# Kernel optimization log

Hardware: AMD Instinct MI355X
Metric: run time of the kernel (lower is better)

The kernel has to match this reference:

```python
import jax, jax.numpy as jnp
import numpy as np

B, S, D = 2, 2048, 2048
NH, NKV, HD = 16, 4, 128
REP = NH // NKV
EPS = 1e-6
ROPE_THETA = 1e6


def setup_inputs() -> dict:
    key = jax.random.key(0)
    ks = jax.random.split(key, 6)
    x = jax.random.normal(ks[0], (B, S, D), jnp.float32)
    # real rotary embeddings: [S, HD]
    inv_freq = 1.0 / (ROPE_THETA ** (np.arange(0, HD, 2, dtype=np.float64) / HD))
    freqs = np.outer(np.arange(S, dtype=np.float64), inv_freq)
    emb = np.concatenate([freqs, freqs], axis=-1)
    cos = jnp.asarray(np.cos(emb), jnp.float32)
    sin = jnp.asarray(np.sin(emb), jnp.float32)
    scale = 1.0 / np.sqrt(D)
    Wq = jax.random.normal(ks[1], (D, NH * HD), jnp.float32) * scale   # [in, out]
    Wk = jax.random.normal(ks[2], (D, NKV * HD), jnp.float32) * scale
    Wv = jax.random.normal(ks[3], (D, NKV * HD), jnp.float32) * scale
    Wo = jax.random.normal(ks[4], (NH * HD, D), jnp.float32) * (1.0 / np.sqrt(NH * HD))
    q_norm_w = jnp.ones((HD,), jnp.float32)
    k_norm_w = jnp.ones((HD,), jnp.float32)
    return dict(x=x, cos=cos, sin=sin, Wq=Wq, Wk=Wk, Wv=Wv, Wo=Wo,
                q_norm_w=q_norm_w, k_norm_w=k_norm_w)


def _rms_norm(h, w):
    var = jnp.mean(h * h, axis=-1, keepdims=True)
    return w * (h * jax.lax.rsqrt(var + EPS))


def _rotate_half(h):
    h1, h2 = jnp.split(h, 2, axis=-1)
    return jnp.concatenate([-h2, h1], axis=-1)


def reference(x, cos, sin, Wq, Wk, Wv, Wo, q_norm_w, k_norm_w):
    b, s, _ = x.shape
    q = (x @ Wq).reshape(b, s, NH, HD)
    k = (x @ Wk).reshape(b, s, NKV, HD)
    v = (x @ Wv).reshape(b, s, NKV, HD)
    # per-head QK RMSNorm
    q = _rms_norm(q, q_norm_w)
    k = _rms_norm(k, k_norm_w)
    # RoPE: cos/sin [S,HD] -> broadcast over batch and heads
    c = cos[None, :, None, :]
    s_ = sin[None, :, None, :]
    q = q * c + _rotate_half(q) * s_
    k = k * c + _rotate_half(k) * s_
    # GQA: group q heads per kv head instead of materializing repeat_kv
    qg = q.reshape(b, s, NKV, REP, HD)
    scores = jnp.einsum('bqgrd,bkgd->bgrqk', qg, k) / np.sqrt(HD)
    causal = jnp.tril(jnp.ones((s, s), bool))  # [q,k]
    scores = jnp.where(causal, scores, -jnp.inf)
    probs = jax.nn.softmax(scores.astype(jnp.float32), axis=-1).astype(q.dtype)
    out = jnp.einsum('bgrqk,bkgd->bqgrd', probs, v).reshape(b, s, NH * HD)
    return out @ Wo
```

## Files before the change

kernel.cpp:

```cpp
#include <hip/hip_runtime.h>
#include <hip/hip_bf16.h>
#include <math.h>

#define B_ 2
#define S_ 2048
#define D_ 2048
#define NH_ 16
#define NKV_ 4
#define HD_ 128
#define EPS_ 1e-6f
#define SCALE_ 0.08838834764831845f
#define LOG2E_ 1.4426950408889634f
#define KOFF_ 2048
#define VOFF_ 2560

typedef float f32x4 __attribute__((ext_vector_type(4)));
typedef short bf16x8 __attribute__((ext_vector_type(8)));
typedef short short4v __attribute__((ext_vector_type(4)));
typedef float float4v __attribute__((ext_vector_type(4)));
typedef unsigned uint2v __attribute__((ext_vector_type(2)));
typedef unsigned uint4v __attribute__((ext_vector_type(4)));

static __device__ __forceinline__ short f2bf(float f) {
    union { float f; unsigned u; } x{f};
    unsigned r = (x.u + 0x7fff + ((x.u >> 16) & 1)) >> 16;
    return (short)r;
}
static __device__ __forceinline__ float bf2f(short s) {
    union { unsigned u; float f; } x; x.u = ((unsigned)(unsigned short)s) << 16; return x.f;
}
static __device__ __forceinline__ unsigned pack_bf2(float a, float b) {
    return __builtin_amdgcn_perm(__builtin_bit_cast(unsigned, b),
                                 __builtin_bit_cast(unsigned, a), 0x07060302u);
}

#define AS1(p) ((const __attribute__((address_space(1))) void*)(p))
#define AS3(p) ((__attribute__((address_space(3))) void*)(p))
static __device__ __forceinline__ void async16(const void* g, void* l) {
    __builtin_amdgcn_global_load_lds(AS1(g), AS3(l), 16, 0, 0);
}

__global__ __launch_bounds__(256) void cast_kernel(const float* __restrict__ in,
                                                   short* __restrict__ out) {
    size_t i = ((size_t)blockIdx.x * 256 + threadIdx.x) * 4;
    float4v v = *(const float4v*)(in + i);
    short4v o; o.x = f2bf(v.x); o.y = f2bf(v.y); o.z = f2bf(v.z); o.w = f2bf(v.w);
    *(short4v*)(out + i) = o;
}

__global__ __launch_bounds__(256) void transpose_all_kernel(const float* __restrict__ Wq,
                                                            const float* __restrict__ Wk,
                                                            const float* __restrict__ Wv,
                                                            const float* __restrict__ Wo,
                                                            short* __restrict__ Wt,
                                                            short* __restrict__ Wot) {
    __shared__ float tile[64][65];
    const int bx = blockIdx.x, by = blockIdx.y;
    const float* src; short* dst; int N, nb;
    if (bx < 32)      { src = Wq; dst = Wt;                         N = 2048; nb = bx; }
    else if (bx < 40) { src = Wk; dst = Wt + (size_t)KOFF_ * 2048;  N = 512;  nb = bx - 32; }
    else if (bx < 48) { src = Wv; dst = Wt + (size_t)VOFF_ * 2048;  N = 512;  nb = bx - 40; }
    else              { src = Wo; dst = Wot;                        N = 2048; nb = bx - 48; }
    const int n0 = nb * 64, k0 = by * 64;
    const int tid = threadIdx.x;
    for (int r = 0; r < 16; ++r) {
        int k = r * 4 + (tid >> 6);
        int n = tid & 63;
        tile[k][n] = src[(size_t)(k0 + k) * N + n0 + n];
    }
    __syncthreads();
    for (int r = 0; r < 4; ++r) {
        int n  = r * 16 + (tid >> 4);
        int kk = (tid & 15) * 4;
        short4v o4;
        o4.x = f2bf(tile[kk + 0][n]); o4.y = f2bf(tile[kk + 1][n]);
        o4.z = f2bf(tile[kk + 2][n]); o4.w = f2bf(tile[kk + 3][n]);
        *(short4v*)&dst[(size_t)(n0 + n) * 2048 + k0 + kk] = o4;
    }
}

template<typename TC>
__global__ __launch_bounds__(256) void gemm_tt_kernel(const short* __restrict__ A,
                                                      const short* __restrict__ Bt,
                                                      TC* __restrict__ C,
                                                      int M, int N, int K) {
    __shared__ short As[128 * 32];
    __shared__ short Bs[128 * 32];

    const int tid  = threadIdx.x;
    const int bn   = blockIdx.x, bm = blockIdx.y;
    const int wave = tid >> 6, lane = tid & 63;
    const int quad = lane >> 4, l16 = lane & 15;
    const int wr = wave >> 1, wc = wave & 1;

    f32x4 acc[4][4];
    for (int i = 0; i < 4; ++i)
        for (int j = 0; j < 4; ++j) acc[i][j] = (f32x4){0.f, 0.f, 0.f, 0.f};

    const short* Abase = A  + (size_t)(bm * 128) * K;
    const short* Bbase = Bt + (size_t)(bn * 128) * K;

    int ci0 = wave * 128 + lane;
    for (int k0 = 0; k0 < K; k0 += 32) {
        __syncthreads();
        for (int t = 0; t < 2; ++t) {
            int ci = ci0 + t * 64;
            int r  = ci >> 2;
            int c  = ((ci & 3) - (r >> 1)) & 3;
            size_t goff = (size_t)r * K + k0 + c * 8;
            async16(Abase + goff, &As[ci * 8]);
            async16(Bbase + goff, &Bs[ci * 8]);
        }
        __syncthreads();

        bf16x8 af[4], bfv[4];
        for (int mt = 0; mt < 4; ++mt) {
            int r = wr * 64 + mt * 16 + l16;
            af[mt] = *(const bf16x8*)&As[r * 32 + (((quad + (r >> 1)) & 3) * 8)];
        }
        for (int nt = 0; nt < 4; ++nt) {
            int r = wc * 64 + nt * 16 + l16;
            bfv[nt] = *(const bf16x8*)&Bs[r * 32 + (((quad + (r >> 1)) & 3) * 8)];
        }
        for (int mt = 0; mt < 4; ++mt)
            for (int nt = 0; nt < 4; ++nt)
                acc[mt][nt] = __builtin_amdgcn_mfma_f32_16x16x32_bf16(
                    af[mt], bfv[nt], acc[mt][nt], 0, 0, 0);
    }

    for (int mt = 0; mt < 4; ++mt)
        for (int nt = 0; nt < 4; ++nt)
            for (int j = 0; j < 4; ++j) {
                int row = bm * 128 + wr * 64 + mt * 16 + quad * 4 + j;
                int col = bn * 128 + wc * 64 + nt * 16 + l16;
                float v = acc[mt][nt][j];
                if constexpr (__is_same(TC, short))
                    C[(size_t)row * N + col] = f2bf(v);
                else
                    C[(size_t)row * N + col] = v;
            }
}

#define QKV_ITERS 16

__global__ __launch_bounds__(512, 2) void qkv_fused_kernel(const short* __restrict__ xb,
                                                           const short* __restrict__ Wt,
                                                           const float* __restrict__ cosb,
                                                           const float* __restrict__ sinb,
                                                           const float* __restrict__ qw,
                                                           const float* __restrict__ kw,
                                                           short* __restrict__ q_rope,
                                                           short* __restrict__ k_rope,
                                                           short* __restrict__ vtr) {
    __shared__ __align__(16) short smem[65536];
    __shared__ float ss2[4][256];

    short* A0 = smem;
    short* A1 = smem + 16384;
    short* B0 = smem + 32768;
    short* B1 = smem + 49152;

    const int tid  = threadIdx.x;
    const int orig = blockIdx.y * 12 + blockIdx.x;
    const int swz  = (orig & 7) * 24 + (orig >> 3);
    const int bn = swz % 12, bm = swz / 12;
    const int wave = tid >> 6, lane = tid & 63;
    const int quad = lane >> 4, l16 = lane & 15;
    const int wr = wave >> 2, wc = wave & 3;

    const short* Ag = xb + (size_t)(bm * 256) * 2048;
    const short* Bg = Wt + (size_t)(bn * 256) * 2048;

    f32x4 acc[8][4];
#pragma unroll
    for (int i = 0; i < 8; ++i)
#pragma unroll
        for (int j = 0; j < 4; ++j) acc[i][j] = (f32x4){0.f, 0.f, 0.f, 0.f};

    bf16x8 a[4][2], b0[2][2], b1[2][2];

    auto stage_half = [&](const short* gpanel, int t, int h, short* lslot) {
#pragma unroll
        for (int u = 0; u < 2; ++u) {
            int ci = u * 512 + tid;
            int r  = ci >> 3;
            int cb = ((ci & 7) * 16) ^ ((r & 7) << 4);
            async16(gpanel + (size_t)(h * 128 + r) * 2048 + t * 64 + (cb >> 1),
                    lslot + h * 8192 + ci * 8);
        }
    };

#define LDA_(lbuf, qm) \
    _Pragma("unroll") for (int mt = 0; mt < 4; ++mt) \
    _Pragma("unroll") for (int ks = 0; ks < 2; ++ks) { \
        int row_ = wr * 128 + (qm) * 64 + mt * 16 + l16; \
        int cb_  = (ks * 64 + quad * 16) ^ ((row_ & 7) << 4); \
        a[mt][ks] = *(const bf16x8*)&(lbuf)[row_ * 64 + (cb_ >> 1)]; \
    }
#define LDB_(lbuf, qn, breg) \
    _Pragma("unroll") for (int ntl = 0; ntl < 2; ++ntl) \
    _Pragma("unroll") for (int ks = 0; ks < 2; ++ks) { \
        int row_ = wc * 64 + (qn) * 32 + ntl * 16 + l16; \
        int cb_  = (ks * 64 + quad * 16) ^ ((row_ & 7) << 4); \
        breg[ntl][ks] = *(const bf16x8*)&(lbuf)[row_ * 64 + (cb_ >> 1)]; \
    }
#define MFMA16_(qm, qn, breg) \
    _Pragma("unroll") for (int mt = 0; mt < 4; ++mt) \
    _Pragma("unroll") for (int ntl = 0; ntl < 2; ++ntl) \
    _Pragma("unroll") for (int ks = 0; ks < 2; ++ks) \
        acc[(qm) * 4 + mt][(qn) * 2 + ntl] = __builtin_amdgcn_mfma_f32_16x16x32_bf16( \
            a[mt][ks], breg[ntl][ks], acc[(qm) * 4 + mt][(qn) * 2 + ntl], 0, 0, 0);
#define PH_BAR() do { __builtin_amdgcn_sched_barrier(0); __builtin_amdgcn_s_barrier(); } while (0)
#define PH_MFMA2(qm) do { \
        __builtin_amdgcn_s_setprio(1); MFMA16_(qm, 0, b0); MFMA16_(qm, 1, b1); \
        __builtin_amdgcn_s_setprio(0); \
        __builtin_amdgcn_sched_barrier(0); __builtin_amdgcn_s_barrier(); } while (0)

    stage_half(Bg, 0, 0, B0); stage_half(Bg, 0, 1, B0);
    stage_half(Ag, 0, 0, A0); stage_half(Ag, 0, 1, A0);
    stage_half(Bg, 1, 0, B1); stage_half(Bg, 1, 1, B1);
    asm volatile("s_waitcnt vmcnt(4)" ::: "memory");
    __builtin_amdgcn_s_barrier();

#pragma unroll 1
    for (int i = 0; i < QKV_ITERS; ++i) {
        const int tE = 2 * i, tO = 2 * i + 1;
        const bool more = (i < QKV_ITERS - 1);

        LDA_(A0, 0); LDB_(B0, 0, b0); LDB_(B0, 1, b1);
        stage_half(Ag, tO, 0, A1); stage_half(Ag, tO, 1, A1);
        PH_BAR();
        PH_MFMA2(0);

        LDA_(A0, 1);
        if (more) {
            stage_half(Bg, tE + 2, 0, B0); stage_half(Bg, tE + 2, 1, B0);
            asm volatile("s_waitcnt vmcnt(4)" ::: "memory");
        } else {
            asm volatile("s_waitcnt vmcnt(0)" ::: "memory");
        }
        PH_BAR();
        PH_MFMA2(1);

        LDA_(A1, 0); LDB_(B1, 0, b0); LDB_(B1, 1, b1);
        if (more) { stage_half(Ag, tE + 2, 0, A0); stage_half(Ag, tE + 2, 1, A0); }
        PH_BAR();
        PH_MFMA2(0);

        LDA_(A1, 1);
        if (more) {
            stage_half(Bg, tO + 2, 0, B1); stage_half(Bg, tO + 2, 1, B1);
            asm volatile("s_waitcnt vmcnt(4)" ::: "memory");
        }
        PH_BAR();
        PH_MFMA2(1);
    }

    if (bn >= 10) {
        const int gbase = (bn - 10) * 2;
#pragma unroll
        for (int am = 0; am < 8; ++am) {
            int tok0 = bm * 256 + wr * 128 + am * 16 + quad * 4;
            int bb = tok0 >> 11, s0 = tok0 & (S_ - 1);
#pragma unroll
            for (int nt = 0; nt < 4; ++nt) {
                int col = wc * 64 + nt * 16 + l16;
                int g = gbase + (col >> 7);
                int d = col & 127;
                short4v o4;
                o4.x = f2bf(acc[am][nt][0]); o4.y = f2bf(acc[am][nt][1]);
                o4.z = f2bf(acc[am][nt][2]); o4.w = f2bf(acc[am][nt][3]);
                *(short4v*)&vtr[((size_t)(bb * NKV_ + g) * HD_ + d) * S_ + s0] = o4;
            }
        }
        return;
    }

    {
        float pss[8][4];
#pragma unroll
        for (int am = 0; am < 8; ++am)
#pragma unroll
            for (int j = 0; j < 4; ++j) {
                float s = 0.f;
#pragma unroll
                for (int nt = 0; nt < 4; ++nt) s += acc[am][nt][j] * acc[am][nt][j];
                pss[am][j] = s;
            }
#pragma unroll
        for (int off = 1; off < 16; off <<= 1)
#pragma unroll
            for (int am = 0; am < 8; ++am)
#pragma unroll
                for (int j = 0; j < 4; ++j)
                    pss[am][j] += __shfl_xor(pss[am][j], off);
        if (l16 == 0)
#pragma unroll
            for (int am = 0; am < 8; ++am)
#pragma unroll
                for (int j = 0; j < 4; ++j)
                    ss2[wc][wr * 128 + am * 16 + quad * 4 + j] = pss[am][j];
    }
    short* ct = smem;
#pragma unroll
    for (int am = 0; am < 8; ++am)
#pragma unroll
        for (int nt = 0; nt < 4; ++nt)
#pragma unroll
            for (int j = 0; j < 4; ++j)
                ct[(wr * 128 + am * 16 + quad * 4 + j) * 256 + wc * 64 + nt * 16 + l16]
                    = f2bf(acc[am][nt][j]);
    __syncthreads();

    const bool isQ = (bn < 8);
    const float osc = isQ ? (SCALE_ * LOG2E_) : 1.0f;
    const float* w = isQ ? qw : kw;
#pragma unroll 1
    for (int it = 0; it < 16; ++it) {
        int idx = it * 512 + tid;
        int row = idx >> 5;
        int s32 = idx & 31;
        int head = s32 >> 4, seg = s32 & 15;
        int tok = bm * 256 + row;
        int bb = tok >> 11, s = tok & (S_ - 1);
        float rstd = rsqrtf((ss2[2 * head][row] + ss2[2 * head + 1][row]) * (1.0f / HD_) + EPS_);
        int c0 = seg * 8, p0 = (seg ^ 8) * 8;
        bf16x8 ta = *(const bf16x8*)&ct[row * 256 + head * 128 + c0];
        bf16x8 tb = *(const bf16x8*)&ct[row * 256 + head * 128 + p0];
        float sgn = (seg < 8) ? -1.0f : 1.0f;
        float4v cs0 = *(const float4v*)&cosb[(size_t)s * HD_ + c0];
        float4v cs1 = *(const float4v*)&cosb[(size_t)s * HD_ + c0 + 4];
        float4v sn0 = *(const float4v*)&sinb[(size_t)s * HD_ + c0];
        float4v sn1 = *(const float4v*)&sinb[(size_t)s * HD_ + c0 + 4];
        float ov[8];
#pragma unroll
        for (int i = 0; i < 8; ++i) {
            float n1 = bf2f(ta[i]) * rstd * w[c0 + i];
            float n2 = bf2f(tb[i]) * rstd * w[p0 + i];
            float cs = (i < 4) ? cs0[i & 3] : cs1[i & 3];
            float sn = (i < 4) ? sn0[i & 3] : sn1[i & 3];
            ov[i] = (n1 * cs + sgn * n2 * sn) * osc;
        }
        uint4v wv;
#pragma unroll
        for (int i2 = 0; i2 < 4; ++i2)
            wv[i2] = ((unsigned)(unsigned short)f2bf(ov[2 * i2])) |
                     ((unsigned)(unsigned short)f2bf(ov[2 * i2 + 1]) << 16);
        int gh = isQ ? (bn * 2 + head) : ((bn - 8) * 2 + head);
        short* dst = isQ
            ? q_rope + ((size_t)(bb * S_ + s) * NH_ + gh) * HD_ + c0
            : k_rope + ((size_t)(bb * NKV_ + gh) * S_ + s) * HD_ + c0;
        *(uint4v*)dst = wv;
    }
#undef LDA_
#undef LDB_
#undef MFMA16_
#undef PH_BAR
#undef PH_MFMA2
}

__global__ __launch_bounds__(256, 2) void attn_kernel(const short* __restrict__ qr,
                                                      const short* __restrict__ kg,
                                                      const short* __restrict__ vt,
                                                      short* __restrict__ aout) {
    __shared__ short Ks[2][64 * 128];
    __shared__ short Vs[2][128 * 64];

    const int lin = blockIdx.x;
    const int b  = lin & 1;
    const int g  = (lin >> 1) & 3;
    const int hq = (lin >> 3) & 3;
    const int pr = lin >> 5;
    const int h  = g * 4 + hq;

    const int wave = threadIdx.x >> 6, lane = threadIdx.x & 63;
    const int quad = lane >> 4, l16 = lane & 15;

    const short* kbase = kg + (size_t)(b * NKV_ + g) * S_ * HD_;
    const short* vbase = vt + (size_t)(b * NKV_ + g) * HD_ * S_;

    for (int pass = 0; pass < 2; ++pass) {
        const int qt    = pass ? (31 - pr) : pr;
        const int iters = qt + 1;
        const int qrow  = qt * 64 + wave * 16 + l16;

        bf16x8 qf[4];
        {
            const short* qp = qr + ((size_t)(b * S_ + qrow) * NH_ + h) * HD_;
            for (int ks = 0; ks < 4; ++ks)
                qf[ks] = *(const bf16x8*)(qp + ks * 32 + quad * 8);
        }

        f32x4 o[8];
        for (int i = 0; i < 8; ++i) o[i] = (f32x4){0.f, 0.f, 0.f, 0.f};
        float m_i = -INFINITY, l_i = 0.f;

        auto stage = [&](int kt, int bsel) {
            const short* kt_base = kbase + (size_t)kt * 64 * HD_;
            const short* vt_base = vbase + kt * 64;
            for (int t = 0; t < 4; ++t) {
                int ci  = (wave * 4 + t) * 64 + lane;
                int key = ci >> 4;
                int c   = (ci & 15) ^ ((key ^ (key >> 2)) & 15);
                async16(kt_base + key * HD_ + c * 8, &Ks[bsel][ci * 8]);
            }
            for (int t = 0; t < 4; ++t) {
                int ci = (wave * 4 + t) * 64 + lane;
                int d  = ci >> 3;
                int c  = (ci & 7) ^ (d & 7);
                async16(vt_base + (size_t)d * S_ + c * 8, &Vs[bsel][ci * 8]);
            }
        };

        stage(0, 0);
        int buf = 0;
        for (int kt = 0; kt < iters; ++kt) {
            __syncthreads();
            if (kt + 1 < iters) stage(kt + 1, buf ^ 1);

            f32x4 acc[4];
            for (int t = 0; t < 4; ++t) acc[t] = (f32x4){0.f, 0.f, 0.f, 0.f};
            __builtin_amdgcn_s_setprio(1);
            for (int t = 0; t < 4; ++t) {
                int lk = ((t >> 1) << 5) + ((l16 >> 2) << 3) + ((t & 1) << 2) + (l16 & 3);
                const short* kp = &Ks[buf][lk * 128];
                int pm = (lk ^ (lk >> 2)) & 15;
                for (int ks = 0; ks < 4; ++ks) {
                    bf16x8 kf = *(const bf16x8*)(kp + (((ks * 4 + quad) ^ pm) * 8));
                    acc[t] = __builtin_amdgcn_mfma_f32_16x16x32_bf16(kf, qf[ks], acc[t], 0, 0, 0);
                }
            }
            __builtin_amdgcn_s_setprio(0);
            const int key_base = kt * 64;
            if (key_base + 63 > qt * 64 + wave * 16) {
                for (int t = 0; t < 4; ++t)
                    for (int j = 0; j < 4; ++j) {
                        int kl = key_base + ((t >> 1) << 5) + (quad << 3) + ((t & 1) << 2) + j;
                        if (kl > qrow) acc[t][j] = -INFINITY;
                    }
            }
            float mx = m_i;
            for (int t = 0; t < 4; ++t)
                for (int j = 0; j < 4; ++j) mx = fmaxf(mx, acc[t][j]);
            mx = fmaxf(mx, __shfl_xor(mx, 16));
            mx = fmaxf(mx, __shfl_xor(mx, 32));
            float al = __builtin_amdgcn_exp2f(m_i - mx);
            m_i = mx;
            float rs = 0.f;
            float p[4][4];
            for (int t = 0; t < 4; ++t)
                for (int j = 0; j < 4; ++j) {
                    float e = __builtin_amdgcn_exp2f(acc[t][j] - mx);
                    p[t][j] = e;
                    rs += e;
                }
            rs += __shfl_xor(rs, 16);
            rs += __shfl_xor(rs, 32);
            l_i = al * l_i + rs;
            for (int d8 = 0; d8 < 8; ++d8)
                for (int j = 0; j < 4; ++j) o[d8][j] *= al;
            unsigned pk[2][4];
            for (int grp = 0; grp < 2; ++grp) {
                pk[grp][0] = pack_bf2(p[2 * grp][0],     p[2 * grp][1]);
                pk[grp][1] = pack_bf2(p[2 * grp][2],     p[2 * grp][3]);
                pk[grp][2] = pack_bf2(p[2 * grp + 1][0], p[2 * grp + 1][1]);
                pk[grp][3] = pack_bf2(p[2 * grp + 1][2], p[2 * grp + 1][3]);
            }
            __builtin_amdgcn_s_setprio(1);
            for (int grp = 0; grp < 2; ++grp) {
                union { unsigned u[4]; bf16x8 v; } pb;
                for (int i = 0; i < 4; ++i) pb.u[i] = pk[grp][i];
                for (int d8 = 0; d8 < 8; ++d8) {
                    int d = d8 * 16 + l16;
                    bf16x8 vf = *(const bf16x8*)&Vs[buf][d * 64 + (((grp * 4 + quad) ^ (d & 7)) * 8)];
                    o[d8] = __builtin_amdgcn_mfma_f32_16x16x32_bf16(vf, pb.v, o[d8], 0, 0, 0);
                }
            }
            __builtin_amdgcn_s_setprio(0);
            buf ^= 1;
        }
        float il = 1.0f / l_i;
        short* op = aout + ((size_t)(b * S_ + qrow) * NH_ + h) * HD_ + quad * 4;
        for (int d8 = 0; d8 < 8; ++d8) {
            uint2v wv;
            wv.x = ((unsigned)(unsigned short)f2bf(o[d8][0] * il)) |
                   ((unsigned)(unsigned short)f2bf(o[d8][1] * il) << 16);
            wv.y = ((unsigned)(unsigned short)f2bf(o[d8][2] * il)) |
                   ((unsigned)(unsigned short)f2bf(o[d8][3] * il) << 16);
            *(uint2v*)(op + d8 * 16) = wv;
        }
        __syncthreads();
    }
}

extern "C" void kernel_launch(void* const* d_in, const int* in_sizes, int n_in,
                              void* d_out, int out_size, void* d_ws, size_t ws_size,
                              hipStream_t stream) {
    (void)in_sizes; (void)n_in; (void)out_size; (void)ws_size;
    const float* x    = (const float*)d_in[0];
    const float* cosb = (const float*)d_in[1];
    const float* sinb = (const float*)d_in[2];
    const float* Wq   = (const float*)d_in[3];
    const float* Wk   = (const float*)d_in[4];
    const float* Wv   = (const float*)d_in[5];
    const float* Wo   = (const float*)d_in[6];
    const float* qw   = (const float*)d_in[7];
    const float* kw   = (const float*)d_in[8];
    float* out = (float*)d_out;

    char* ws = (char*)d_ws;
    short* xb     = (short*)ws;  ws += (size_t)4096 * 2048 * 2;
    short* Wt     = (short*)ws;  ws += (size_t)3072 * 2048 * 2;
    short* Wot    = (short*)ws;  ws += (size_t)2048 * 2048 * 2;
    short* q_rope = (short*)ws;  ws += (size_t)4096 * 2048 * 2;
    short* k_rope = (short*)ws;  ws += (size_t)4096 * 512 * 2;
    short* vt     = (short*)ws;  ws += (size_t)4096 * 512 * 2;
    short* a_out  = (short*)ws;  ws += (size_t)4096 * 2048 * 2;

    const int M = B_ * S_;

    cast_kernel<<<M * 2048 / 1024, 256, 0, stream>>>(x, xb);
    transpose_all_kernel<<<dim3(80, 32), 256, 0, stream>>>(Wq, Wk, Wv, Wo, Wt, Wot);

    qkv_fused_kernel<<<dim3(12, M / 256), 512, 0, stream>>>(
        xb, Wt, cosb, sinb, qw, kw, q_rope, k_rope, vt);

    attn_kernel<<<512, 256, 0, stream>>>(q_rope, k_rope, vt, a_out);

    gemm_tt_kernel<float><<<dim3(D_ / 128, M / 128), 256, 0, stream>>>(
        a_out, Wot, out, M, D_, 2048);
}
```

Measured before the change: 304.2 us.

## Pipeline output projection GEMM with double-buffered LDS and trim QKV barriers

Replaces the simple synchronous output-projection GEMM with a 512-thread, 128x256-tile kernel. It double-buffers swizzled LDS tiles loaded asynchronously, uses phased MFMA groups with priority boosts, and remaps blocks with a swizzle for L2 reuse. The QKV kernel's schedule is also reordered so global-to-LDS staging is issued before fragment loads, and the separate barrier before each MFMA phase is dropped, leaving one barrier per phase. The aim is to hide memory latency and cut synchronisation, at the cost of more LDS per block and tighter vmcnt bookkeeping that could allow races if miscounted.

```diff
diff --git a/kernel.cpp b/kernel.cpp
--- a/kernel.cpp
+++ b/kernel.cpp
@@ -39,6 +39,7 @@
 static __device__ __forceinline__ void async16(const void* g, void* l) {
     __builtin_amdgcn_global_load_lds(AS1(g), AS3(l), 16, 0, 0);
 }
+#define SB_() __builtin_amdgcn_sched_barrier(0)
 
 __global__ __launch_bounds__(256) void cast_kernel(const float* __restrict__ in,
                                                    short* __restrict__ out) {
@@ -79,66 +80,114 @@
     }
 }
 
-template<typename TC>
-__global__ __launch_bounds__(256) void gemm_tt_kernel(const short* __restrict__ A,
-                                                      const short* __restrict__ Bt,
-                                                      TC* __restrict__ C,
-                                                      int M, int N, int K) {
-    __shared__ short As[128 * 32];
-    __shared__ short Bs[128 * 32];
+__global__ __launch_bounds__(512, 2) void gemm_oproj_kernel(const short* __restrict__ A,
+                                                            const short* __restrict__ Bt,
+                                                            float* __restrict__ C) {
+    __shared__ __align__(16) short smem[49152];
+    short* A0 = smem;
+    short* A1 = smem + 8192;
+    short* B0 = smem + 16384;
+    short* B1 = smem + 32768;
 
     const int tid  = threadIdx.x;
-    const int bn   = blockIdx.x, bm = blockIdx.y;
+    const int orig = blockIdx.y * 8 + blockIdx.x;
+    const int swz  = (orig & 7) * 32 + (orig >> 3);
+    const int bn = swz & 7, bm = swz >> 3;
     const int wave = tid >> 6, lane = tid & 63;
     const int quad = lane >> 4, l16 = lane & 15;
-    const int wr = wave >> 1, wc = wave & 1;
+    const int wr = wave >> 2, wc = wave & 3;
+
+    const short* Ag = A  + (size_t)(bm * 128) * 2048;
+    const short* Bg = Bt + (size_t)(bn * 256) * 2048;
 
     f32x4 acc[4][4];
+#pragma unroll
     for (int i = 0; i < 4; ++i)
+#pragma unroll
         for (int j = 0; j < 4; ++j) acc[i][j] = (f32x4){0.f, 0.f, 0.f, 0.f};
 
-    const short* Abase = A  + (size_t)(bm * 128) * K;
-    const short* Bbase = Bt + (size_t)(bn * 128) * K;
-
-    int ci0 = wave * 128 + lane;
-    for (int k0 = 0; k0 < K; k0 += 32) {
-        __syncthreads();
-        for (int t = 0; t < 2; ++t) {
-            int ci = ci0 + t * 64;
-            int r  = ci >> 2;
-            int c  = ((ci & 3) - (r >> 1)) & 3;
-            size_t goff = (size_t)r * K + k0 + c * 8;
-            async16(Abase + goff, &As[ci * 8]);
-            async16(Bbase + goff, &Bs[ci * 8]);
-        }
-        __syncthreads();
-
-        bf16x8 af[4], bfv[4];
-        for (int mt = 0; mt < 4; ++mt) {
-            int r = wr * 64 + mt * 16 + l16;
-            af[mt] = *(const bf16x8*)&As[r * 32 + (((quad + (r >> 1)) & 3) * 8)];
-        }
-        for (int nt = 0; nt < 4; ++nt) {
-            int r = wc * 64 + nt * 16 + l16;
-            bfv[nt] = *(const bf16x8*)&Bs[r * 32 + (((quad + (r >> 1)) & 3) * 8)];
-        }
-        for (int mt = 0; mt < 4; ++mt)
-            for (int nt = 0; nt < 4; ++nt)
-                acc[mt][nt] = __builtin_amdgcn_mfma_f32_16x16x32_bf16(
-                    af[mt], bfv[nt], acc[mt][nt], 0, 0, 0);
-    }
-
+    bf16x8 a[4][2], b0[2][2], b1[2][2];
+
+    auto stage_half = [&](const short* gpanel, int t, int h, short* lslot) {
+#pragma unroll
+        for (int u = 0; u < 2; ++u) {
+            int ci = u * 512 + tid;
+            int r  = ci >> 3;
+            int cb = ((ci & 7) * 16) ^ ((r & 7) << 4);
+            async16(gpanel + (size_t)(h * 128 + r) * 2048 + t * 64 + (cb >> 1),
+                    lslot + h * 8192 + ci * 8);
+        }
+    };
+
+#define OLDA_(lbuf) \
+    _Pragma("unroll") for (int mt = 0; mt < 4; ++mt) \
+    _Pragma("unroll") for (int ks = 0; ks < 2; ++ks) { \
+        int row_ = wr * 64 + mt * 16 + l16; \
+        int cb_  = (ks * 64 + quad * 16) ^ ((row_ & 7) << 4); \
+        a[mt][ks] = *(const bf16x8*)&(lbuf)[row_ * 64 + (cb_ >> 1)]; \
+    }
+#define OLDB_(lbuf, qn, breg) \
+    _Pragma("unroll") for (int ntl = 0; ntl < 2; ++ntl) \
+    _Pragma("unroll") for (int ks = 0; ks < 2; ++ks) { \
+        int row_ = wc * 64 + (qn) * 32 + ntl * 16 + l16; \
+        int cb_  = (ks * 64 + quad * 16) ^ ((row_ & 7) << 4); \
+        breg[ntl][ks] = *(const bf16x8*)&(lbuf)[row_ * 64 + (cb_ >> 1)]; \
+    }
+#define OMFMA_(qn, breg) do { \
+    __builtin_amdgcn_s_setprio(1); \
+    _Pragma("unroll") for (int mt = 0; mt < 4; ++mt) \
+    _Pragma("unroll") for (int ntl = 0; ntl < 2; ++ntl) \
+    _Pragma("unroll") for (int ks = 0; ks < 2; ++ks) \
+        acc[mt][(qn) * 2 + ntl] = __builtin_amdgcn_mfma_f32_16x16x32_bf16( \
+            a[mt][ks], breg[ntl][ks], acc[mt][(qn) * 2 + ntl], 0, 0, 0); \
+    __builtin_amdgcn_s_setprio(0); SB_(); __builtin_amdgcn_s_barrier(); } while (0)
+
+    stage_half(Bg, 0, 0, B0); stage_half(Bg, 0, 1, B0);
+    stage_half(Ag, 0, 0, A0);
+    SB_(); asm volatile("s_waitcnt vmcnt(0)" ::: "memory");
+    __builtin_amdgcn_s_barrier();
+
+#pragma unroll 1
+    for (int i = 0; i < 16; ++i) {
+        const int tE = 2 * i, tO = 2 * i + 1;
+        const bool more = (i < 15);
+
+        stage_half(Ag, tO, 0, A1);
+        stage_half(Bg, tO, 0, B1); stage_half(Bg, tO, 1, B1);
+        OLDA_(A0); OLDB_(B0, 0, b0);
+        OMFMA_(0, b0);
+
+        if (more) {
+            stage_half(Ag, tE + 2, 0, A0);
+            SB_(); asm volatile("s_waitcnt vmcnt(2)" ::: "memory");
+        } else {
+            SB_(); asm volatile("s_waitcnt vmcnt(0)" ::: "memory");
+        }
+        OLDB_(B0, 1, b1);
+        OMFMA_(1, b1);
+
+        if (more) { stage_half(Bg, tE + 2, 0, B0); stage_half(Bg, tE + 2, 1, B0); }
+        OLDA_(A1); OLDB_(B1, 0, b0);
+        OMFMA_(0, b0);
+
+        if (more) { SB_(); asm volatile("s_waitcnt vmcnt(0)" ::: "memory"); }
+        OLDB_(B1, 1, b1);
+        OMFMA_(1, b1);
+    }
+
+#pragma unroll
     for (int mt = 0; mt < 4; ++mt)
+#pragma unroll
         for (int nt = 0; nt < 4; ++nt)
+#pragma unroll
             for (int j = 0; j < 4; ++j) {
                 int row = bm * 128 + wr * 64 + mt * 16 + quad * 4 + j;
-                int col = bn * 128 + wc * 64 + nt * 16 + l16;
-                float v = acc[mt][nt][j];
-                if constexpr (__is_same(TC, short))
-                    C[(size_t)row * N + col] = f2bf(v);
-                else
-                    C[(size_t)row * N + col] = v;
-            }
+                int col = bn * 256 + wc * 64 + nt * 16 + l16;
+                C[(size_t)row * 2048 + col] = acc[mt][nt][j];
+            }
+#undef OLDA_
+#undef OLDB_
+#undef OMFMA_
 }
 
 #define QKV_ITERS 16
@@ -210,16 +259,14 @@
     _Pragma("unroll") for (int ks = 0; ks < 2; ++ks) \
         acc[(qm) * 4 + mt][(qn) * 2 + ntl] = __builtin_amdgcn_mfma_f32_16x16x32_bf16( \
             a[mt][ks], breg[ntl][ks], acc[(qm) * 4 + mt][(qn) * 2 + ntl], 0, 0, 0);
-#define PH_BAR() do { __builtin_amdgcn_sched_barrier(0); __builtin_amdgcn_s_barrier(); } while (0)
-#define PH_MFMA2(qm) do { \
+#define PH_MFMA2_(qm) do { \
         __builtin_amdgcn_s_setprio(1); MFMA16_(qm, 0, b0); MFMA16_(qm, 1, b1); \
-        __builtin_amdgcn_s_setprio(0); \
-        __builtin_amdgcn_sched_barrier(0); __builtin_amdgcn_s_barrier(); } while (0)
+        __builtin_amdgcn_s_setprio(0); SB_(); __builtin_amdgcn_s_barrier(); } while (0)
 
     stage_half(Bg, 0, 0, B0); stage_half(Bg, 0, 1, B0);
     stage_half(Ag, 0, 0, A0); stage_half(Ag, 0, 1, A0);
     stage_half(Bg, 1, 0, B1); stage_half(Bg, 1, 1, B1);
-    asm volatile("s_waitcnt vmcnt(4)" ::: "memory");
+    SB_(); asm volatile("s_waitcnt vmcnt(4)" ::: "memory");
     __builtin_amdgcn_s_barrier();
 
 #pragma unroll 1
@@ -227,33 +274,29 @@
         const int tE = 2 * i, tO = 2 * i + 1;
         const bool more = (i < QKV_ITERS - 1);
 
+        stage_half(Ag, tO, 0, A1); stage_half(Ag, tO, 1, A1);
         LDA_(A0, 0); LDB_(B0, 0, b0); LDB_(B0, 1, b1);
-        stage_half(Ag, tO, 0, A1); stage_half(Ag, tO, 1, A1);
-        PH_BAR();
-        PH_MFMA2(0);
-
-        LDA_(A0, 1);
+        PH_MFMA2_(0);
+
         if (more) {
             stage_half(Bg, tE + 2, 0, B0); stage_half(Bg, tE + 2, 1, B0);
-            asm volatile("s_waitcnt vmcnt(4)" ::: "memory");
+            SB_(); asm volatile("s_waitcnt vmcnt(4)" ::: "memory");
         } else {
-            asm volatile("s_waitcnt vmcnt(0)" ::: "memory");
-        }
-        PH_BAR();
-        PH_MFMA2(1);
-
+            SB_(); asm volatile("s_waitcnt vmcnt(0)" ::: "memory");
+        }
+        LDA_(A0, 1);
+        PH_MFMA2_(1);
+
+        if (more) { stage_half(Ag, tE + 2, 0, A0); stage_half(Ag, tE + 2, 1, A0); }
         LDA_(A1, 0); LDB_(B1, 0, b0); LDB_(B1, 1, b1);
-        if (more) { stage_half(Ag, tE + 2, 0, A0); stage_half(Ag, tE + 2, 1, A0); }
-        PH_BAR();
-        PH_MFMA2(0);
-
-        LDA_(A1, 1);
+        PH_MFMA2_(0);
+
         if (more) {
             stage_half(Bg, tO + 2, 0, B1); stage_half(Bg, tO + 2, 1, B1);
-            asm volatile("s_waitcnt vmcnt(4)" ::: "memory");
-        }
-        PH_BAR();
-        PH_MFMA2(1);
+            SB_(); asm volatile("s_waitcnt vmcnt(4)" ::: "memory");
+        }
+        LDA_(A1, 1);
+        PH_MFMA2_(1);
     }
 
     if (bn >= 10) {
@@ -355,8 +398,7 @@
 #undef LDA_
 #undef LDB_
 #undef MFMA16_
-#undef PH_BAR
-#undef PH_MFMA2
+#undef PH_MFMA2_
 }
 
 __global__ __launch_bounds__(256, 2) void attn_kernel(const short* __restrict__ qr,
@@ -527,6 +569,5 @@
 
     attn_kernel<<<512, 256, 0, stream>>>(q_rope, k_rope, vt, a_out);
 
-    gemm_tt_kernel<float><<<dim3(D_ / 128, M / 128), 256, 0, stream>>>(
-        a_out, Wot, out, M, D_, 2048);
-}
+    gemm_oproj_kernel<<<dim3(8, 32), 512, 0, stream>>>(a_out, Wot, out);
+}
```

Result: faster. 292.6 us (-3.8%).
